# Kernel tuning notes

Measured on AMD Instinct MI355X. Metric: run time of the kernel, lower is better.

Reference implementation:

```python
import jax, jax.numpy as jnp
import numpy as np

N_NODES = 50000
N_EDGES = 800000
LEAKY_SLOPE = 0.25


def setup_inputs() -> dict:
    key = jax.random.key(0)
    ks = jax.random.split(key, 12)
    in_dim, h = 512, [256, 256, 128, 128]
    x = jax.random.normal(ks[0], (N_NODES, in_dim), dtype=jnp.float32)
    row = jax.random.randint(ks[1], (N_EDGES,), 0, N_NODES, dtype=jnp.int32)
    col = jax.random.randint(ks[2], (N_EDGES,), 0, N_NODES, dtype=jnp.int32)
    vals = jax.random.uniform(ks[3], (N_EDGES,), dtype=jnp.float32)
    def xavier(k, fan_in, fan_out):
        std = np.sqrt(2.0 / (fan_in + fan_out))
        return jax.random.normal(k, (fan_in, fan_out), dtype=jnp.float32) * std
    W1 = xavier(ks[4], in_dim, h[0]); b1 = jnp.zeros((h[0],), jnp.float32)
    W2 = xavier(ks[5], h[0], h[1]);  b2 = jnp.zeros((h[1],), jnp.float32)
    W3 = xavier(ks[6], h[1], h[2]);  b3 = jnp.zeros((h[2],), jnp.float32)
    W4 = xavier(ks[7], h[2], h[3]);  b4 = jnp.zeros((h[3],), jnp.float32)
    return {"x": x, "row": row, "col": col, "vals": vals,
            "W1": W1, "b1": b1, "W2": W2, "b2": b2,
            "W3": W3, "b3": b3, "W4": W4, "b4": b4}


def _gconv(x, row, col, vals, W, b):
    # support = x @ W  (dense transform), then SpMM: out[i] = sum_e vals[e] * support[col[e]] for row[e]==i
    support = x @ W
    msgs = support[col] * vals[:, None]           # [E, out_dim] gather + edge-weight
    out = jax.ops.segment_sum(msgs, row, num_segments=x.shape[0])  # scatter-add
    return out + b


def reference(x, row, col, vals, W1, b1, W2, b2, W3, b3, W4, b4):
    lrelu = lambda t: jnp.where(t >= 0, t, LEAKY_SLOPE * t)
    # dropout is identity in eval mode (deterministic reference)
    h = lrelu(_gconv(x, row, col, vals, W1, b1))
    h = lrelu(_gconv(h, row, col, vals, W2, b2))
    h = lrelu(_gconv(h, row, col, vals, W3, b3))
    h = lrelu(_gconv(h, row, col, vals, W4, b4))
    return h
```

## Files before the change

kernel.cpp:

```cpp
#include <hip/hip_runtime.h>
#include <hip/hip_bf16.h>

#define NN 50000
#define NE 800000
#define LEAKY 0.25f
#define SCAN_NB ((NN + 255) / 256)

typedef __attribute__((ext_vector_type(8))) short bf16x8;
typedef __attribute__((ext_vector_type(8))) ushort u16x8;
typedef __attribute__((ext_vector_type(4))) float f32x4;
typedef unsigned long long ull;

static __device__ __forceinline__ ushort f2bf(float f) {
    union { __hip_bfloat16 h; ushort u; } cv;
    cv.h = __float2bfloat16(f);
    return cv.u;
}
static __device__ __forceinline__ float bf2f(ushort u) {
    union { unsigned u; float f; } cv;
    cv.u = ((unsigned)u) << 16;
    return cv.f;
}

__global__ void cast_bf16_x8(const float4* __restrict__ in, u16x8* __restrict__ out, int n8) {
    int i = blockIdx.x * blockDim.x + threadIdx.x;
    if (i >= n8) return;
    float4 v0 = in[i * 2];
    float4 v1 = in[i * 2 + 1];
    u16x8 o;
    o[0] = f2bf(v0.x); o[1] = f2bf(v0.y); o[2] = f2bf(v0.z); o[3] = f2bf(v0.w);
    o[4] = f2bf(v1.x); o[5] = f2bf(v1.y); o[6] = f2bf(v1.z); o[7] = f2bf(v1.w);
    out[i] = o;
}

__global__ void cast_transpose_w(const float* __restrict__ W, ushort* __restrict__ Wt, int K, int N) {
    int idx = blockIdx.x * blockDim.x + threadIdx.x;
    if (idx >= K * N) return;
    int k = idx / N, n = idx % N;
    Wt[n * K + k] = f2bf(W[idx]);
}

template<int BN>
__global__ __launch_bounds__(256) void gemm_bf16(
    const ushort* __restrict__ A, const ushort* __restrict__ Bt,
    ushort* __restrict__ C, int M, int K)
{
    constexpr int NI = BN / 32;
    constexpr int BPASS = BN / 64;
    __shared__ ushort As[64 * 32];
    __shared__ ushort Bs[BN * 32];
    const int tid  = threadIdx.x;
    const int lane = tid & 63;
    const int wid  = tid >> 6;
    const int wr = wid >> 1, wc = wid & 1;
    const int m0 = blockIdx.x * 64;

    int ar = m0 + (tid >> 2); if (ar >= M) ar = M - 1;
    const int ccol = (tid & 3) * 8;

    const ushort* gA = A + (size_t)ar * K + ccol;
    const ushort* gB[BPASS];
    #pragma unroll
    for (int p = 0; p < BPASS; ++p)
        gB[p] = Bt + (size_t)(p * 64 + (tid >> 2)) * K + ccol;

    char* ldsA = (char*)As + wid * 1024;
    char* ldsB = (char*)Bs + wid * 1024;

    const int fr = lane & 15;
    const int fq = lane >> 4;

    const ushort* fragA = As + (wr * 32 + fr) * 32 + fq * 8;
    const ushort* fragB = Bs + (wc * (BN / 2) + fr) * 32 + fq * 8;

    f32x4 acc[2][NI];
    #pragma unroll
    for (int i = 0; i < 2; ++i)
        #pragma unroll
        for (int j = 0; j < NI; ++j)
            acc[i][j] = {0.f, 0.f, 0.f, 0.f};

    for (int k0 = 0; k0 < K; k0 += 32) {
        __builtin_amdgcn_global_load_lds((const __attribute__((address_space(1))) void*)(gA + k0),
                                         (__attribute__((address_space(3))) void*)(ldsA), 16, 0, 0);
        #pragma unroll
        for (int p = 0; p < BPASS; ++p)
            __builtin_amdgcn_global_load_lds((const __attribute__((address_space(1))) void*)(gB[p] + k0),
                                             (__attribute__((address_space(3))) void*)(ldsB + p * 4096), 16, 0, 0);
        __syncthreads();

        bf16x8 a[2], b[NI];
        #pragma unroll
        for (int mi = 0; mi < 2; ++mi) a[mi] = *(const bf16x8*)(fragA + mi * 16 * 32);
        #pragma unroll
        for (int ni = 0; ni < NI; ++ni) b[ni] = *(const bf16x8*)(fragB + ni * 16 * 32);
        #pragma unroll
        for (int mi = 0; mi < 2; ++mi)
            #pragma unroll
            for (int ni = 0; ni < NI; ++ni)
                acc[mi][ni] = __builtin_amdgcn_mfma_f32_16x16x32_bf16(a[mi], b[ni], acc[mi][ni], 0, 0, 0);
        __syncthreads();
    }

    #pragma unroll
    for (int mi = 0; mi < 2; ++mi) {
        #pragma unroll
        for (int j = 0; j < 4; ++j) {
            int row = m0 + wr * 32 + mi * 16 + fq * 4 + j;
            if (row >= M) continue;
            #pragma unroll
            for (int ni = 0; ni < NI; ++ni) {
                int colg = wc * (BN / 2) + ni * 16 + fr;
                C[(size_t)row * BN + colg] = f2bf(acc[mi][ni][j]);
            }
        }
    }
}

__global__ void hist_rows(const int* __restrict__ row, int* __restrict__ cnt) {
    int e = blockIdx.x * blockDim.x + threadIdx.x;
    if (e < NE) atomicAdd(&cnt[row[e]], 1);
}

__global__ void scan_bsum(const int* __restrict__ cnt, int* __restrict__ bsum) {
    int i = blockIdx.x * 256 + threadIdx.x;
    int v = (i < NN) ? cnt[i] : 0;
    #pragma unroll
    for (int off = 32; off >= 1; off >>= 1) v += __shfl_down(v, off);
    __shared__ int ws[4];
    if ((threadIdx.x & 63) == 0) ws[threadIdx.x >> 6] = v;
    __syncthreads();
    if (threadIdx.x == 0) bsum[blockIdx.x] = ws[0] + ws[1] + ws[2] + ws[3];
}

__global__ void scan_boff(const int* __restrict__ bsum, int* __restrict__ boff,
                          int* __restrict__ rowptr) {
    __shared__ int s[256];
    int t = threadIdx.x;
    int v = (t < SCAN_NB) ? bsum[t] : 0;
    s[t] = v;
    __syncthreads();
    #pragma unroll
    for (int off = 1; off < 256; off <<= 1) {
        int u = (t >= off) ? s[t - off] : 0;
        __syncthreads();
        s[t] += u;
        __syncthreads();
    }
    if (t < SCAN_NB) boff[t] = s[t] - v;
    if (t == 255) rowptr[NN] = s[255];
}

__global__ void scan_write(const int* __restrict__ cnt, const int* __restrict__ boff,
                           int* __restrict__ rowptr, int* __restrict__ rowcur) {
    __shared__ int s[256];
    int b = blockIdx.x;
    int t = threadIdx.x;
    int i = b * 256 + t;
    int v = (i < NN) ? cnt[i] : 0;
    s[t] = v;
    __syncthreads();
    #pragma unroll
    for (int off = 1; off < 256; off <<= 1) {
        int u = (t >= off) ? s[t - off] : 0;
        __syncthreads();
        s[t] += u;
        __syncthreads();
    }
    if (i < NN) {
        int ex = boff[b] + s[t] - v;
        rowptr[i] = ex;
        rowcur[i] = ex;
    }
}

__global__ void scatter_edges(const int* __restrict__ row, const int* __restrict__ col,
                              const float* __restrict__ vals,
                              int* __restrict__ rowcur,
                              ull* __restrict__ epack) {
    int e = blockIdx.x * blockDim.x + threadIdx.x;
    if (e < NE) {
        int p = atomicAdd(&rowcur[row[e]], 1);
        ull pk = ((ull)__float_as_uint(vals[e]) << 32) | (unsigned)col[e];
        epack[p] = pk;
    }
}

template<int DIM, bool OUT_BF16>
__global__ __launch_bounds__(256) void spmm_gather_bf16(
    const ushort* __restrict__ support,
    const int* __restrict__ rowptr,
    const ull* __restrict__ epack,
    const float* __restrict__ bias,
    void* __restrict__ out) {
    constexpr int LPR = DIM / 8;
    constexpr int RPB = 256 / LPR;
    int r = blockIdx.x * RPB + threadIdx.x / LPR;
    int lane = threadIdx.x % LPR;
    if (r >= NN) return;
    int s = rowptr[r], e = rowptr[r + 1];
    float acc0[8] = {}, acc1[8] = {};
    int i = s;
    for (; i + 3 < e; i += 4) {
        ull p0 = epack[i];
        ull p1 = epack[i + 1];
        ull p2 = epack[i + 2];
        ull p3 = epack[i + 3];
        u16x8 v0 = *((const u16x8*)(support + (size_t)(unsigned)p0 * DIM) + lane);
        u16x8 v1 = *((const u16x8*)(support + (size_t)(unsigned)p1 * DIM) + lane);
        u16x8 v2 = *((const u16x8*)(support + (size_t)(unsigned)p2 * DIM) + lane);
        u16x8 v3 = *((const u16x8*)(support + (size_t)(unsigned)p3 * DIM) + lane);
        float w0 = __uint_as_float((unsigned)(p0 >> 32));
        float w1 = __uint_as_float((unsigned)(p1 >> 32));
        float w2 = __uint_as_float((unsigned)(p2 >> 32));
        float w3 = __uint_as_float((unsigned)(p3 >> 32));
        #pragma unroll
        for (int j = 0; j < 8; ++j) acc0[j] += w0 * bf2f(v0[j]);
        #pragma unroll
        for (int j = 0; j < 8; ++j) acc1[j] += w1 * bf2f(v1[j]);
        #pragma unroll
        for (int j = 0; j < 8; ++j) acc0[j] += w2 * bf2f(v2[j]);
        #pragma unroll
        for (int j = 0; j < 8; ++j) acc1[j] += w3 * bf2f(v3[j]);
    }
    for (; i < e; ++i) {
        ull p0 = epack[i];
        float w0 = __uint_as_float((unsigned)(p0 >> 32));
        u16x8 v0 = *((const u16x8*)(support + (size_t)(unsigned)p0 * DIM) + lane);
        #pragma unroll
        for (int j = 0; j < 8; ++j) acc0[j] += w0 * bf2f(v0[j]);
    }
    const float4 bb0 = ((const float4*)bias)[lane * 2];
    const float4 bb1 = ((const float4*)bias)[lane * 2 + 1];
    float acc[8];
    #pragma unroll
    for (int j = 0; j < 8; ++j) acc[j] = acc0[j] + acc1[j];
    acc[0] += bb0.x; acc[1] += bb0.y; acc[2] += bb0.z; acc[3] += bb0.w;
    acc[4] += bb1.x; acc[5] += bb1.y; acc[6] += bb1.z; acc[7] += bb1.w;
    #pragma unroll
    for (int j = 0; j < 8; ++j) acc[j] = (acc[j] >= 0.f) ? acc[j] : LEAKY * acc[j];
    if (OUT_BF16) {
        ushort4 o0, o1;
        o0.x = f2bf(acc[0]); o0.y = f2bf(acc[1]); o0.z = f2bf(acc[2]); o0.w = f2bf(acc[3]);
        o1.x = f2bf(acc[4]); o1.y = f2bf(acc[5]); o1.z = f2bf(acc[6]); o1.w = f2bf(acc[7]);
        ((ushort4*)out)[(size_t)r * LPR * 2 + lane * 2]     = o0;
        ((ushort4*)out)[(size_t)r * LPR * 2 + lane * 2 + 1] = o1;
    } else {
        float4 f0 = {acc[0], acc[1], acc[2], acc[3]};
        float4 f1 = {acc[4], acc[5], acc[6], acc[7]};
        ((float4*)out)[(size_t)r * LPR * 2 + lane * 2]     = f0;
        ((float4*)out)[(size_t)r * LPR * 2 + lane * 2 + 1] = f1;
    }
}

extern "C" void kernel_launch(void* const* d_in, const int* in_sizes, int n_in,
                              void* d_out, int out_size, void* d_ws, size_t ws_size,
                              hipStream_t stream) {
    const float* x    = (const float*)d_in[0];
    const int*   row  = (const int*)d_in[1];
    const int*   col  = (const int*)d_in[2];
    const float* vals = (const float*)d_in[3];
    const float* W1 = (const float*)d_in[4];  const float* b1 = (const float*)d_in[5];
    const float* W2 = (const float*)d_in[6];  const float* b2 = (const float*)d_in[7];
    const float* W3 = (const float*)d_in[8];  const float* b3 = (const float*)d_in[9];
    const float* W4 = (const float*)d_in[10]; const float* b4 = (const float*)d_in[11];

    ushort* Xb = (ushort*)d_ws;
    ushort* Hb = Xb;
    ushort* S  = Xb + (size_t)NN * 512;
    ushort* Wt1 = S + (size_t)NN * 256;
    ushort* Wt2 = Wt1 + 512 * 256;
    ushort* Wt3 = Wt2 + 256 * 256;
    ushort* Wt4 = Wt3 + 256 * 128;
    int* cnt    = (int*)(Wt4 + 128 * 128);
    int* rowptr = cnt + NN;
    int* rowcur = rowptr + (NN + 1);
    int* pend   = rowcur + (NN + 1);
    ull* epack  = (ull*)pend;
    int* bsum   = (int*)(epack + NE);
    int* boff   = bsum + SCAN_NB;
    float* out  = (float*)d_out;

    {
        int n8 = NN * 512 / 8;
        cast_bf16_x8<<<(n8 + 255) / 256, 256, 0, stream>>>((const float4*)x, (u16x8*)Xb, n8);
        cast_transpose_w<<<(512 * 256 + 255) / 256, 256, 0, stream>>>(W1, Wt1, 512, 256);
        cast_transpose_w<<<(256 * 256 + 255) / 256, 256, 0, stream>>>(W2, Wt2, 256, 256);
        cast_transpose_w<<<(256 * 128 + 255) / 256, 256, 0, stream>>>(W3, Wt3, 256, 128);
        cast_transpose_w<<<(128 * 128 + 255) / 256, 256, 0, stream>>>(W4, Wt4, 128, 128);
    }

    hipMemsetAsync(cnt, 0, NN * sizeof(int), stream);
    hist_rows<<<(NE + 255) / 256, 256, 0, stream>>>(row, cnt);
    scan_bsum<<<SCAN_NB, 256, 0, stream>>>(cnt, bsum);
    scan_boff<<<1, 256, 0, stream>>>(bsum, boff, rowptr);
    scan_write<<<SCAN_NB, 256, 0, stream>>>(cnt, boff, rowptr, rowcur);
    scatter_edges<<<(NE + 255) / 256, 256, 0, stream>>>(row, col, vals, rowcur, epack);

    const int MT64 = (NN + 63) / 64;

    gemm_bf16<256><<<MT64, 256, 0, stream>>>(Xb, Wt1, S, NN, 512);
    spmm_gather_bf16<256, true><<<(NN + 7) / 8, 256, 0, stream>>>(S, rowptr, epack, b1, Hb);
    gemm_bf16<256><<<MT64, 256, 0, stream>>>(Hb, Wt2, S, NN, 256);
    spmm_gather_bf16<256, true><<<(NN + 7) / 8, 256, 0, stream>>>(S, rowptr, epack, b2, Hb);
    gemm_bf16<128><<<MT64, 256, 0, stream>>>(Hb, Wt3, S, NN, 256);
    spmm_gather_bf16<128, true><<<(NN + 15) / 16, 256, 0, stream>>>(S, rowptr, epack, b3, Hb);
    gemm_bf16<128><<<MT64, 256, 0, stream>>>(Hb, Wt4, S, NN, 128);
    spmm_gather_bf16<128, false><<<(NN + 15) / 16, 256, 0, stream>>>(S, rowptr, epack, b4, out);
}
```

Before: 378.2 us.

## Double-buffer GEMM LDS tiles and merge weight cast kernels into one launch

The bf16 GEMM now keeps two LDS buffers, so the global-to-LDS load for the next K tile is issued while MFMAs run on the current tile. This drops one barrier per iteration and is meant to hide load latency. The four weight cast/transpose launches are folded into a single kernel to cut launch overhead. LDS use doubles, which may reduce occupancy for the BN=256 variant. Correctness relies on the single barrier at the top of each iteration ordering reuse of the alternate buffer.

```diff
diff --git a/kernel.cpp b/kernel.cpp
--- a/kernel.cpp
+++ b/kernel.cpp
@@ -10,6 +10,9 @@
 typedef __attribute__((ext_vector_type(8))) ushort u16x8;
 typedef __attribute__((ext_vector_type(4))) float f32x4;
 typedef unsigned long long ull;
+
+#define AS1 const __attribute__((address_space(1))) void*
+#define AS3 __attribute__((address_space(3))) void*
 
 static __device__ __forceinline__ ushort f2bf(float f) {
     union { __hip_bfloat16 h; ushort u; } cv;
@@ -33,11 +36,20 @@
     out[i] = o;
 }
 
-__global__ void cast_transpose_w(const float* __restrict__ W, ushort* __restrict__ Wt, int K, int N) {
+__global__ void cast_transpose_all(const float* __restrict__ W1, const float* __restrict__ W2,
+                                   const float* __restrict__ W3, const float* __restrict__ W4,
+                                   ushort* __restrict__ Wt1, ushort* __restrict__ Wt2,
+                                   ushort* __restrict__ Wt3, ushort* __restrict__ Wt4) {
     int idx = blockIdx.x * blockDim.x + threadIdx.x;
-    if (idx >= K * N) return;
-    int k = idx / N, n = idx % N;
-    Wt[n * K + k] = f2bf(W[idx]);
+    const float* W; ushort* Wt; int K, N, base;
+    if (idx < 131072)      { W = W1; Wt = Wt1; K = 512; N = 256; base = 0; }
+    else if (idx < 196608) { W = W2; Wt = Wt2; K = 256; N = 256; base = 131072; }
+    else if (idx < 229376) { W = W3; Wt = Wt3; K = 256; N = 128; base = 196608; }
+    else if (idx < 245760) { W = W4; Wt = Wt4; K = 128; N = 128; base = 229376; }
+    else return;
+    int l = idx - base;
+    int k = l / N, n = l % N;
+    Wt[n * K + k] = f2bf(W[l]);
 }
 
 template<int BN>
@@ -47,8 +59,10 @@
 {
     constexpr int NI = BN / 32;
     constexpr int BPASS = BN / 64;
-    __shared__ ushort As[64 * 32];
-    __shared__ ushort Bs[BN * 32];
+    constexpr int ASZ = 64 * 32;
+    constexpr int BSZ = BN * 32;
+    __shared__ ushort As[2 * ASZ];
+    __shared__ ushort Bs[2 * BSZ];
     const int tid  = threadIdx.x;
     const int lane = tid & 63;
     const int wid  = tid >> 6;
@@ -64,14 +78,17 @@
     for (int p = 0; p < BPASS; ++p)
         gB[p] = Bt + (size_t)(p * 64 + (tid >> 2)) * K + ccol;
 
-    char* ldsA = (char*)As + wid * 1024;
-    char* ldsB = (char*)Bs + wid * 1024;
-
     const int fr = lane & 15;
     const int fq = lane >> 4;
 
-    const ushort* fragA = As + (wr * 32 + fr) * 32 + fq * 8;
-    const ushort* fragB = Bs + (wc * (BN / 2) + fr) * 32 + fq * 8;
+    auto STAGE = [&](int buf, int k0) {
+        char* lA = (char*)(As + buf * ASZ) + wid * 1024;
+        char* lB = (char*)(Bs + buf * BSZ) + wid * 1024;
+        __builtin_amdgcn_global_load_lds((AS1)(gA + k0), (AS3)lA, 16, 0, 0);
+        #pragma unroll
+        for (int p = 0; p < BPASS; ++p)
+            __builtin_amdgcn_global_load_lds((AS1)(gB[p] + k0), (AS3)(lB + p * 4096), 16, 0, 0);
+    };
 
     f32x4 acc[2][NI];
     #pragma unroll
@@ -80,15 +97,15 @@
         for (int j = 0; j < NI; ++j)
             acc[i][j] = {0.f, 0.f, 0.f, 0.f};
 
-    for (int k0 = 0; k0 < K; k0 += 32) {
-        __builtin_amdgcn_global_load_lds((const __attribute__((address_space(1))) void*)(gA + k0),
-                                         (__attribute__((address_space(3))) void*)(ldsA), 16, 0, 0);
-        #pragma unroll
-        for (int p = 0; p < BPASS; ++p)
-            __builtin_amdgcn_global_load_lds((const __attribute__((address_space(1))) void*)(gB[p] + k0),
-                                             (__attribute__((address_space(3))) void*)(ldsB + p * 4096), 16, 0, 0);
-        __syncthreads();
-
+    STAGE(0, 0);
+    const int nk = K >> 5;
+    for (int t = 0; t < nk; ++t) {
+        const int cur = t & 1;
+        __syncthreads();
+        if (t + 1 < nk) STAGE(cur ^ 1, (t + 1) << 5);
+
+        const ushort* fragA = As + cur * ASZ + (wr * 32 + fr) * 32 + fq * 8;
+        const ushort* fragB = Bs + cur * BSZ + (wc * (BN / 2) + fr) * 32 + fq * 8;
         bf16x8 a[2], b[NI];
         #pragma unroll
         for (int mi = 0; mi < 2; ++mi) a[mi] = *(const bf16x8*)(fragA + mi * 16 * 32);
@@ -99,7 +116,6 @@
             #pragma unroll
             for (int ni = 0; ni < NI; ++ni)
                 acc[mi][ni] = __builtin_amdgcn_mfma_f32_16x16x32_bf16(a[mi], b[ni], acc[mi][ni], 0, 0, 0);
-        __syncthreads();
     }
 
     #pragma unroll
@@ -284,10 +300,7 @@
     {
         int n8 = NN * 512 / 8;
         cast_bf16_x8<<<(n8 + 255) / 256, 256, 0, stream>>>((const float4*)x, (u16x8*)Xb, n8);
-        cast_transpose_w<<<(512 * 256 + 255) / 256, 256, 0, stream>>>(W1, Wt1, 512, 256);
-        cast_transpose_w<<<(256 * 256 + 255) / 256, 256, 0, stream>>>(W2, Wt2, 256, 256);
-        cast_transpose_w<<<(256 * 128 + 255) / 256, 256, 0, stream>>>(W3, Wt3, 256, 128);
-        cast_transpose_w<<<(128 * 128 + 255) / 256, 256, 0, stream>>>(W4, Wt4, 128, 128);
+        cast_transpose_all<<<(245760 + 255) / 256, 256, 0, stream>>>(W1, W2, W3, W4, Wt1, Wt2, Wt3, Wt4);
     }
 
     hipMemsetAsync(cnt, 0, NN * sizeof(int), stream);
```

Result: no change. 373.6 us (median of 2 runs) (-1.2%).
